# Optimization experiments

Measured on AMD Instinct MI355X. Metric: run time of the kernel, lower is better.

The kernel has to match this reference:

```python
import jax, jax.numpy as jnp
import numpy as np
from jax import lax

K = 4
OUT_PLANES = 128
TEMPERATURE = 30.0


def setup_inputs() -> dict:
    key = jax.random.key(0)
    ks = jax.random.split(key, 5)
    in_planes, k = 128, 3
    he_std = float(np.sqrt(2.0)) * (in_planes * k * k) ** (-0.5)
    return {
        "x": jax.random.normal(ks[0], (16, in_planes, 64, 64), jnp.float32),
        "weight": jax.random.normal(ks[1], (K * OUT_PLANES, in_planes, k, k), jnp.float32) * he_std,
        "bias": jax.random.normal(ks[2], (K * OUT_PLANES,), jnp.float32) * 0.01,
        "se_w1": jax.random.normal(ks[3], (33, in_planes), jnp.float32) * (2.0 / 33) ** 0.5,
        "se_w2": jax.random.normal(ks[4], (K, 33), jnp.float32) * (2.0 / K) ** 0.5,
        "se_b2": jnp.zeros((K,), jnp.float32),
    }


def reference(x, weight, bias, se_w1, se_w2, se_b2):
    B = x.shape[0]
    # SE attention: global avg pool -> fc1 -> relu -> fc2 -> softmax(./T)
    pooled = x.mean(axis=(2, 3))                      # [B, Cin]
    h = jax.nn.relu(pooled @ se_w1.T)                 # [B, hidden]
    logits = h @ se_w2.T + se_b2                      # [B, K]
    attn = jax.nn.softmax(logits / TEMPERATURE, axis=1)
    # conv with K*out channels (groups=1, stride=1, pad=1, dil=1)
    y = lax.conv_general_dilated(
        x, weight, window_strides=(1, 1), padding=[(1, 1), (1, 1)],
        dimension_numbers=("NCHW", "OIHW", "NCHW"))
    y = y + bias[None, :, None, None]                 # [B, K*out, Ho, Wo]
    Ho, Wo = y.shape[2], y.shape[3]
    y = y.reshape(B, K, OUT_PLANES, Ho, Wo)
    # attention-weighted combine over K branches (bmm in torch)
    return jnp.einsum("bk,bkohw->bohw", attn, y)
```

## Files before the change

### kernel.cpp

```cpp
#include <hip/hip_runtime.h>
#include <cstdint>
#include <cstddef>

typedef unsigned short u16;
typedef __attribute__((ext_vector_type(8))) short short8;
typedef __attribute__((ext_vector_type(4))) float f32x4;

__device__ __forceinline__ u16 f2bf(float f){
  union { float f; unsigned u; } c; c.f = f;
  unsigned u = c.u;
  u += 0x7fffu + ((u >> 16) & 1u);
  return (u16)(u >> 16);
}
__device__ __forceinline__ unsigned pk2(float a, float b){
  union { float f; unsigned u; } ca, cb; ca.f = a; cb.f = b;
  return ((ca.u + 0x8000u) >> 16) | ((cb.u + 0x8000u) & 0xFFFF0000u);
}

#define XB_STRIDE 557568
#define XR_STRIDE 8448


#define GLD_LDS(gsrc, ldst) \
  __builtin_amdgcn_global_load_lds((const __attribute__((address_space(1))) void*)(gsrc), \
                                   (__attribute__((address_space(3))) void*)(ldst), 16, 0, 0)

#define BAR { asm volatile("s_waitcnt lgkmcnt(0)" ::: "memory"); \
              __builtin_amdgcn_s_barrier(); }
#define WAIT_VM(N) asm volatile("s_waitcnt vmcnt(" #N ")" ::: "memory")

__global__ __launch_bounds__(256) void xpose_pool(
    const float* __restrict__ x, u16* __restrict__ xT2, float* __restrict__ part)
{
  const int bid = blockIdx.x;
  const int b = bid & 15, chunk = bid >> 4;
  const int pos0 = chunk << 6;
  const int tid = threadIdx.x;
  __shared__ u16 tile[8192];
  __shared__ float psum[128 * 17];
  const float* xb = x + ((size_t)b << 19) + pos0;
  const int rq = tid & 15;
  const int p4 = rq << 2;
  const int gci = tid >> 4;

  if (chunk == 0){
    u16* xh = xT2 + (size_t)b * XB_STRIDE;
    for (int i = tid; i < 4160; i += 256){
      const int p = i >> 4, oct = i & 15;
      int row, col;
      if (p < 66)      { row = 0;        col = p; }
      else if (p < 132){ row = 65;       col = p - 66; }
      else if (p < 196){ row = p - 131;  col = 0; }
      else             { row = p - 195;  col = 65; }
      *(uint4*)(xh + row * XR_STRIDE + (col << 7) + (oct << 3)) =
          make_uint4(0u, 0u, 0u, 0u);
    }
  }

  {
    const int ci8 = gci << 3;
    float4 L[8];
    #pragma unroll
    for (int j = 0; j < 8; ++j)
      L[j] = *(const float4*)(xb + ((size_t)(ci8 + j) << 12) + p4);
    #pragma unroll
    for (int j = 0; j < 8; ++j)
      psum[(ci8 + j) * 17 + rq] = L[j].x + L[j].y + L[j].z + L[j].w;
    const int gs = gci ^ (rq & 7);
    const float* e = (const float*)L;
    #pragma unroll
    for (int p = 0; p < 4; ++p){
      const int row = p4 + p;
      uint4 V;
      V.x = pk2(e[0 * 4 + p], e[1 * 4 + p]);
      V.y = pk2(e[2 * 4 + p], e[3 * 4 + p]);
      V.z = pk2(e[4 * 4 + p], e[5 * 4 + p]);
      V.w = pk2(e[6 * 4 + p], e[7 * 4 + p]);
      *(uint4*)(tile + (row << 7) + (gs << 3)) = V;
    }
  }
  __syncthreads();

  if (tid < 128){
    float s = 0.f;
    #pragma unroll
    for (int j = 0; j < 16; ++j) s += psum[tid * 17 + j];
    part[(((b << 6) | chunk) << 7) + tid] = s;
  }

  u16* xo = xT2 + (size_t)b * XB_STRIDE;
  const int g = tid & 15, rb = (tid >> 4) << 2;
  #pragma unroll
  for (int r = 0; r < 4; ++r){
    const int row = rb + r;
    const int gs = g ^ ((row >> 2) & 7);
    uint4 v = *(const uint4*)(tile + (row << 7) + (gs << 3));
    const int pos = pos0 + row;
    const int h = pos >> 6, w = pos & 63;
    *(uint4*)(xo + (h + 1) * XR_STRIDE + ((w + 1) << 7) + (g << 3)) = v;
  }
}

__global__ __launch_bounds__(256) void combine(
    const float* __restrict__ W, const float* __restrict__ bias,
    const float* __restrict__ part, const float* __restrict__ w1,
    const float* __restrict__ w2, const float* __restrict__ b2,
    u16* __restrict__ wcomb, float* __restrict__ bcomb)
{
  __shared__ float wlds[9216];
  __shared__ float sp[128];
  __shared__ float sh[33];
  __shared__ float sat[4];
  const int bid = blockIdx.x;
  const int b = bid & 15, cp = bid >> 4;
  const int tid = threadIdx.x;

  #pragma unroll
  for (int it = 0; it < 9; ++it){
    const int G = it * 256 + tid;
    const int k = G / 576, rem = G - k * 576;
    const int co_l = rem / 288, j4 = rem - co_l * 288;
    const float* src = W + (size_t)(k * 128 + (cp << 1) + co_l) * 1152 + (j4 << 2);
    GLD_LDS(src, (char*)wlds + (G << 4));
  }

  if (tid < 128){
    const float* pb = part + (b << 13);
    float s = 0.f;
    #pragma unroll 8
    for (int c = 0; c < 64; ++c) s += pb[(c << 7) + tid];
    sp[tid] = s * (1.f / 4096.f);
  }
  __syncthreads();
  if (tid < 33){
    float h = 0.f;
    for (int ci = 0; ci < 128; ++ci) h += sp[ci] * w1[tid * 128 + ci];
    sh[tid] = fmaxf(h, 0.f);
  }
  __syncthreads();
  if (tid == 0){
    float l[4];
    #pragma unroll
    for (int t = 0; t < 4; ++t){
      float v = b2[t];
      for (int j = 0; j < 33; ++j) v += sh[j] * w2[t * 33 + j];
      l[t] = v * (1.f / 30.f);
    }
    float m = fmaxf(fmaxf(l[0], l[1]), fmaxf(l[2], l[3]));
    float e0 = __expf(l[0] - m), e1 = __expf(l[1] - m);
    float e2 = __expf(l[2] - m), e3 = __expf(l[3] - m);
    float inv = 1.f / (e0 + e1 + e2 + e3);
    sat[0] = e0 * inv; sat[1] = e1 * inv; sat[2] = e2 * inv; sat[3] = e3 * inv;
  }
  asm volatile("s_waitcnt vmcnt(0)" ::: "memory");
  __syncthreads();
  const float a0 = sat[0], a1 = sat[1], a2 = sat[2], a3 = sat[3];

  if (tid < 2){
    const int co = (cp << 1) + tid;
    bcomb[(b << 7) + co] = a0 * bias[co] + a1 * bias[128 + co]
                         + a2 * bias[256 + co] + a3 * bias[384 + co];
  }

  u16* wob = wcomb + (size_t)b * 147456;
  for (int gi = tid; gi < 288; gi += 256){
    const int co_l = gi / 144;
    const int r = gi - co_l * 144;
    const int tap = r >> 4;
    const int gg = r & 15;
    const int q = gg >> 2, g = gg & 3;
    const int co = (cp << 1) + co_l;
    union { u16 h[8]; uint4 v; } pk;
    #pragma unroll
    for (int e = 0; e < 8; ++e){
      const int ci = (q << 5) + (g << 3) + e;
      const int j = ci * 9 + tap;
      float s = a0 * wlds[co_l * 1152 + j]        + a1 * wlds[2304 + co_l * 1152 + j]
              + a2 * wlds[4608 + co_l * 1152 + j] + a3 * wlds[6912 + co_l * 1152 + j];
      pk.h[e] = f2bf(s);
    }
    *(uint4*)(wob + (((tap << 2) + q) << 12) + (co << 5) + (g << 3)) = pk.v;
  }
}

__global__ __launch_bounds__(256, 2) void conv_mfma(
    const u16* __restrict__ xT2, const u16* __restrict__ wcomb,
    const float* __restrict__ bcomb, float* __restrict__ out)
{
  extern __shared__ char smem[];
  u16* s_x = (u16*)smem;
  u16* s_w = (u16*)(smem + 33792);

  const int tid = threadIdx.x;
  const int lane = tid & 63, wid = tid >> 6;
  const int wr = wid & 1, wcv = wid >> 1;
  const int l15 = lane & 15, hi = lane >> 4;

  const int bid = blockIdx.x;
  const int b = bid & 15;
  const int h0 = (bid >> 4) << 1;

  const u16* Abase = wcomb + (size_t)b * 147456;
  const u16* Xbase = xT2 + (size_t)b * XB_STRIDE;

#define STAGE_X(Q) { \
    u16* _sx = s_x + ((Q) & 1) * 8448; \
    _Pragma("unroll") \
    for (int _it = 0; _it < 5; ++_it){ \
      const int _G = _it * 256 + tid; \
      if (_it < 4 || _G < 1056){ \
        const int _oct = _G & 3, _t = _G >> 2; \
        const int _col = _t % 66, _row = _t / 66; \
        const u16* _src = Xbase + (h0 + _row) * XR_STRIDE + (_col << 7) \
                        + ((Q) << 5) + (_oct << 3); \
        GLD_LDS(_src, _sx + (_G << 3)); \
      } \
    } }

#define STAGE_W(Q, TAP, BUF) { \
    const u16* _As = Abase + ((((TAP) << 2) + (Q)) << 12) + (wcv << 11); \
    u16* _sw = s_w + (wid << 12) + ((BUF) << 11); \
    _Pragma("unroll") \
    for (int _it = 0; _it < 4; ++_it){ \
      const int _g = (_it << 6) + lane; \
      GLD_LDS(_As + (_g << 3), _sw + (_g << 3)); \
    } }

#define COMPUTE(Q, TAP, BUF) { \
    const int _dh = (TAP) / 3, _dw = (TAP) - 3 * (_dh); \
    const u16* _sw = s_w + (wid << 12) + ((BUF) << 11); \
    const u16* _sx = s_x + ((Q) & 1) * 8448; \
    short8 _af[4], _bf[4]; \
    _Pragma("unroll") \
    for (int _a = 0; _a < 4; ++_a){ \
      const int _cl = (_a << 4) + l15; \
      _af[_a] = *(const short8*)(_sw + (_cl << 5) + (hi << 3)); \
    } \
    _Pragma("unroll") \
    for (int _p = 0; _p < 4; ++_p){ \
      const int _col = l15 + _dw + (_p << 4); \
      _bf[_p] = *(const short8*)(_sx + (((wr + _dh) * 66 + _col) << 5) + (hi << 3)); \
    } \
    _Pragma("unroll") \
    for (int _a = 0; _a < 4; ++_a) \
      _Pragma("unroll") \
      for (int _p = 0; _p < 4; ++_p) \
        acc[_a][_p] = __builtin_amdgcn_mfma_f32_16x16x32_bf16(_af[_a], _bf[_p], acc[_a][_p], 0, 0, 0); }

  f32x4 acc[4][4] = {};

  STAGE_X(0);
  STAGE_W(0, 0, 0);
  WAIT_VM(0);
  __syncthreads();

  for (int q = 0; q < 4; ++q){
    #pragma unroll
    for (int tap = 0; tap < 9; ++tap){
      const int s = q * 9 + tap;
      if (s < 35){
        const int nq = (tap == 8) ? q + 1 : q;
        const int nt = (tap == 8) ? 0 : tap + 1;
        STAGE_W(nq, nt, (s + 1) & 1);
      }
      if (tap == 5 && q < 3){ STAGE_X(q + 1); }
      if (s == 35)                             { WAIT_VM(0); }
      else if (q < 3 && (tap == 5 || tap == 6)){ WAIT_VM(8); }
      else                                     { WAIT_VM(4); }
      __builtin_amdgcn_s_setprio(1);
      COMPUTE(q, tap, s & 1);
      __builtin_amdgcn_s_setprio(0);
      if (tap == 8 && q < 3){ BAR; }
    }
  }

#undef COMPUTE
#undef STAGE_W
#undef STAGE_X

  const int hrow = h0 + wr;
  float* ob = out + ((size_t)b << 19) + (hrow << 6) + l15;
  #pragma unroll
  for (int a = 0; a < 4; ++a){
    const int co0 = (wcv << 6) + (a << 4) + (hi << 2);
    #pragma unroll
    for (int r = 0; r < 4; ++r){
      const float bc = bcomb[(b << 7) + co0 + r];
      float* op = ob + (size_t)(co0 + r) * 4096;
      #pragma unroll
      for (int p = 0; p < 4; ++p)
        __builtin_nontemporal_store(acc[a][p][r] + bc, op + (p << 4));
    }
  }
}

extern "C" void kernel_launch(void* const* d_in, const int* in_sizes, int n_in,
                              void* d_out, int out_size, void* d_ws, size_t ws_size,
                              hipStream_t stream)
{
  const float* x    = (const float*)d_in[0];
  const float* W    = (const float*)d_in[1];
  const float* bias = (const float*)d_in[2];
  const float* w1   = (const float*)d_in[3];
  const float* w2   = (const float*)d_in[4];
  const float* b2   = (const float*)d_in[5];
  float* out = (float*)d_out;

  char* ws = (char*)d_ws;
  float* part  = (float*)(ws);
  float* bcomb = (float*)(ws + 524288);
  u16*   xT2   = (u16*)  (ws + 532480);
  u16*   wcomb = (u16*)  (ws + 18374656);

  xpose_pool<<<1024, 256, 0, stream>>>(x, xT2, part);
  combine<<<1024, 256, 0, stream>>>(W, bias, part, w1, w2, b2, wcomb, bcomb);

  (void)hipFuncSetAttribute(reinterpret_cast<const void*>(conv_mfma),
                            hipFuncAttributeMaxDynamicSharedMemorySize, 66560);
  conv_mfma<<<512, 256, 66560, stream>>>(xT2, wcomb, bcomb, out);
}
```

Before: 49.61 us.

## Load combined weights directly into registers in MFMA fragment layout, dropping LDS staging

The combine kernel now writes the per-batch combined weights in the exact per-lane MFMA A-fragment order. The conv kernel then loads A fragments straight from global memory into double-buffered registers instead of staging them through LDS with global_load_lds. This halves dynamic shared memory, which may allow more resident blocks, and removes the LDS reads for A. The main loop is fully unrolled with a single wait-and-barrier per input-channel chunk. The risk is that global load latency for A is now exposed in registers with only one step of prefetch, and register pressure rises.

```diff
diff --git a/kernel.cpp b/kernel.cpp
--- a/kernel.cpp
+++ b/kernel.cpp
@@ -179,7 +179,9 @@
               + a2 * wlds[4608 + co_l * 1152 + j] + a3 * wlds[6912 + co_l * 1152 + j];
       pk.h[e] = f2bf(s);
     }
-    *(uint4*)(wob + (((tap << 2) + q) << 12) + (co << 5) + (g << 3)) = pk.v;
+    const int st = q * 9 + tap;
+    *(uint4*)(wob + (st << 12) + ((co >> 6) << 11) + (((co >> 4) & 3) << 9)
+                  + (g << 7) + ((co & 15) << 3)) = pk.v;
   }
 }
 
@@ -189,7 +191,6 @@
 {
   extern __shared__ char smem[];
   u16* s_x = (u16*)smem;
-  u16* s_w = (u16*)(smem + 33792);
 
   const int tid = threadIdx.x;
   const int lane = tid & 63, wid = tid >> 6;
@@ -200,7 +201,7 @@
   const int b = bid & 15;
   const int h0 = (bid >> 4) << 1;
 
-  const u16* Abase = wcomb + (size_t)b * 147456;
+  const u16* Ab = wcomb + (size_t)b * 147456 + (wcv << 11) + (hi << 7) + (l15 << 3);
   const u16* Xbase = xT2 + (size_t)b * XB_STRIDE;
 
 #define STAGE_X(Q) { \
@@ -217,25 +218,17 @@
       } \
     } }
 
-#define STAGE_W(Q, TAP, BUF) { \
-    const u16* _As = Abase + ((((TAP) << 2) + (Q)) << 12) + (wcv << 11); \
-    u16* _sw = s_w + (wid << 12) + ((BUF) << 11); \
-    _Pragma("unroll") \
-    for (int _it = 0; _it < 4; ++_it){ \
-      const int _g = (_it << 6) + lane; \
-      GLD_LDS(_As + (_g << 3), _sw + (_g << 3)); \
-    } }
+#define LOAD_A(S, BUF) { \
+    const u16* _as = Ab + ((S) << 12); \
+    af[BUF][0] = *(const short8*)(_as); \
+    af[BUF][1] = *(const short8*)(_as + 512); \
+    af[BUF][2] = *(const short8*)(_as + 1024); \
+    af[BUF][3] = *(const short8*)(_as + 1536); }
 
 #define COMPUTE(Q, TAP, BUF) { \
     const int _dh = (TAP) / 3, _dw = (TAP) - 3 * (_dh); \
-    const u16* _sw = s_w + (wid << 12) + ((BUF) << 11); \
     const u16* _sx = s_x + ((Q) & 1) * 8448; \
-    short8 _af[4], _bf[4]; \
-    _Pragma("unroll") \
-    for (int _a = 0; _a < 4; ++_a){ \
-      const int _cl = (_a << 4) + l15; \
-      _af[_a] = *(const short8*)(_sw + (_cl << 5) + (hi << 3)); \
-    } \
+    short8 _bf[4]; \
     _Pragma("unroll") \
     for (int _p = 0; _p < 4; ++_p){ \
       const int _col = l15 + _dw + (_p << 4); \
@@ -245,37 +238,33 @@
     for (int _a = 0; _a < 4; ++_a) \
       _Pragma("unroll") \
       for (int _p = 0; _p < 4; ++_p) \
-        acc[_a][_p] = __builtin_amdgcn_mfma_f32_16x16x32_bf16(_af[_a], _bf[_p], acc[_a][_p], 0, 0, 0); }
+        acc[_a][_p] = __builtin_amdgcn_mfma_f32_16x16x32_bf16(af[BUF][_a], _bf[_p], acc[_a][_p], 0, 0, 0); }
 
   f32x4 acc[4][4] = {};
+  short8 af[2][4];
 
   STAGE_X(0);
-  STAGE_W(0, 0, 0);
+  LOAD_A(0, 0);
   WAIT_VM(0);
   __syncthreads();
 
-  for (int q = 0; q < 4; ++q){
-    #pragma unroll
-    for (int tap = 0; tap < 9; ++tap){
-      const int s = q * 9 + tap;
-      if (s < 35){
-        const int nq = (tap == 8) ? q + 1 : q;
-        const int nt = (tap == 8) ? 0 : tap + 1;
-        STAGE_W(nq, nt, (s + 1) & 1);
-      }
-      if (tap == 5 && q < 3){ STAGE_X(q + 1); }
-      if (s == 35)                             { WAIT_VM(0); }
-      else if (q < 3 && (tap == 5 || tap == 6)){ WAIT_VM(8); }
-      else                                     { WAIT_VM(4); }
-      __builtin_amdgcn_s_setprio(1);
-      COMPUTE(q, tap, s & 1);
-      __builtin_amdgcn_s_setprio(0);
-      if (tap == 8 && q < 3){ BAR; }
-    }
-  }
-
+#define STEP(Q, TAP) { \
+    const int _s = (Q) * 9 + (TAP); \
+    if (_s < 35) LOAD_A(_s + 1, ((_s + 1) & 1)); \
+    if ((TAP) == 5 && (Q) < 3) STAGE_X((Q) + 1); \
+    __builtin_amdgcn_s_setprio(1); \
+    COMPUTE(Q, TAP, (_s & 1)); \
+    __builtin_amdgcn_s_setprio(0); \
+    if ((TAP) == 8 && (Q) < 3){ WAIT_VM(0); BAR; } }
+
+  STEP(0,0) STEP(0,1) STEP(0,2) STEP(0,3) STEP(0,4) STEP(0,5) STEP(0,6) STEP(0,7) STEP(0,8)
+  STEP(1,0) STEP(1,1) STEP(1,2) STEP(1,3) STEP(1,4) STEP(1,5) STEP(1,6) STEP(1,7) STEP(1,8)
+  STEP(2,0) STEP(2,1) STEP(2,2) STEP(2,3) STEP(2,4) STEP(2,5) STEP(2,6) STEP(2,7) STEP(2,8)
+  STEP(3,0) STEP(3,1) STEP(3,2) STEP(3,3) STEP(3,4) STEP(3,5) STEP(3,6) STEP(3,7) STEP(3,8)
+
+#undef STEP
 #undef COMPUTE
-#undef STAGE_W
+#undef LOAD_A
 #undef STAGE_X
 
   const int hrow = h0 + wr;
@@ -316,6 +305,6 @@
   combine<<<1024, 256, 0, stream>>>(W, bias, part, w1, w2, b2, wcomb, bcomb);
 
   (void)hipFuncSetAttribute(reinterpret_cast<const void*>(conv_mfma),
-                            hipFuncAttributeMaxDynamicSharedMemorySize, 66560);
-  conv_mfma<<<512, 256, 66560, stream>>>(xT2, wcomb, bcomb, out);
-}
+                            hipFuncAttributeMaxDynamicSharedMemorySize, 33792);
+  conv_mfma<<<512, 256, 33792, stream>>>(xT2, wcomb, bcomb, out);
+}
```

Measured after the change: 47.40 us. 1.05x faster.
